# Kernel tuning notes

Measured on AMD Instinct MI355X. Metric: run time of the kernel, lower is better.

The kernel has to match this reference:

```python
import jax, jax.numpy as jnp
import numpy as np

B, N, E, H = 8, 2048, 1024, 16
D = E // H

def setup_inputs() -> dict:
    key = jax.random.key(0)
    kx, kw1, kb1, kw2, kb2 = jax.random.split(key, 5)
    scale = 0.02
    return {
        "x": jax.random.normal(kx, (B, N, E), dtype=jnp.float32),
        "Wqkv": jax.random.normal(kw1, (3 * E, E), dtype=jnp.float32) * scale,
        "bqkv": jax.random.normal(kb1, (3 * E,), dtype=jnp.float32) * scale,
        "Wo": jax.random.normal(kw2, (E, E), dtype=jnp.float32) * scale,
        "bo": jax.random.normal(kb2, (E,), dtype=jnp.float32) * scale,
    }

def reference(x, Wqkv, bqkv, Wo, bo):
    b, n, e = x.shape
    h, d = H, D
    # qkv projection: torch Linear is x @ W.T + b
    qkv = x @ Wqkv.T + bqkv                                   # [B,N,3E]
    qkv = qkv.reshape(b, n, 3, h, d).transpose(2, 0, 3, 1, 4)  # [3,B,H,N,D]
    q, k, v = qkv[0], qkv[1], qkv[2]                           # each [B,H,N,D]
    # NOTE: replicates the original's einsum labeling exactly: with q,k of
    # shape [B,H,N,D], 'nqhd,nkhd->nhqk' contracts over D and yields [B,N,H,H]
    # (softmax over the head axis), matching the torch source bit-for-bit.
    energy = jnp.einsum('nqhd,nkhd->nhqk', q, k)               # [B,N,H,H]
    attention = jax.nn.softmax(energy / jnp.sqrt(jnp.float32(e)), axis=-1)
    out = jnp.einsum('nhql,nlhd->nqhd', attention, v)          # [B,H,N,D]
    out = out.reshape(b, n, e)                                 # same raw-buffer reshape as torch
    return out @ Wo.T + bo
```

## Files before the change

kernel.cpp:

```cpp
#include <hip/hip_runtime.h>
#include <hip/hip_bf16.h>
#include <stdint.h>


typedef __attribute__((ext_vector_type(8))) short short8;
typedef __attribute__((ext_vector_type(8))) unsigned short ushort8;
typedef __attribute__((ext_vector_type(16))) float floatx16;

__device__ __forceinline__ unsigned short f2bf(float f) {
  union { float f; uint32_t u; } x; x.f = f;
  uint32_t u = x.u;
  return (unsigned short)((u + 0x7fffu + ((u >> 16) & 1u)) >> 16);
}
__device__ __forceinline__ float bf2f(unsigned short s) {
  union { uint32_t u; float f; } x; x.u = ((uint32_t)s) << 16; return x.f;
}
__device__ __forceinline__ void unpack8(uint4 u, float* f) {
  f[0] = bf2f((unsigned short)(u.x & 0xffffu)); f[1] = bf2f((unsigned short)(u.x >> 16));
  f[2] = bf2f((unsigned short)(u.y & 0xffffu)); f[3] = bf2f((unsigned short)(u.y >> 16));
  f[4] = bf2f((unsigned short)(u.z & 0xffffu)); f[5] = bf2f((unsigned short)(u.z >> 16));
  f[6] = bf2f((unsigned short)(u.w & 0xffffu)); f[7] = bf2f((unsigned short)(u.w >> 16));
}

__global__ __launch_bounds__(256) void cvt_all(const float* __restrict__ x,
                                               const float* __restrict__ w1,
                                               const float* __restrict__ w2,
                                               unsigned short* __restrict__ xb,
                                               unsigned short* __restrict__ w1b,
                                               unsigned short* __restrict__ w2b) {
  int i = blockIdx.x * 256 + threadIdx.x;
  const float* src;
  unsigned short* dst;
  if (i < 2097152) {
    src = x; dst = xb;
  } else if (i < 2097152 + 393216) {
    i -= 2097152; src = w1; dst = w1b;
  } else {
    i -= 2490368; src = w2; dst = w2b;
  }
  long base = (long)i * 8;
  const float4* p = (const float4*)(src + base);
  float4 a = p[0], b = p[1];
  ushort8 r;
  r[0] = f2bf(a.x); r[1] = f2bf(a.y); r[2] = f2bf(a.z); r[3] = f2bf(a.w);
  r[4] = f2bf(b.x); r[5] = f2bf(b.y); r[6] = f2bf(b.z); r[7] = f2bf(b.w);
  *(ushort8*)(dst + base) = r;
}

__device__ __forceinline__ void gl2lds16(const void* g, void* l) {
  __builtin_amdgcn_global_load_lds(
      (const uint32_t __attribute__((address_space(1)))*)g,
      (uint32_t __attribute__((address_space(3)))*)(uint32_t)(uintptr_t)l,
      16, 0, 0);
}

template <bool OUT_BF16>
__device__ __forceinline__ void gemm_core(const unsigned short* __restrict__ A,
                                          const unsigned short* __restrict__ Bm,
                                          const float* __restrict__ bias,
                                          void* __restrict__ Cout, int K,
                                          int ncols, int ldc) {
  const int id = blockIdx.x;
  const int local = id % (8 * ncols);
  const int brow = (id / (8 * ncols)) * 8 + (local & 7);
  const int bcol = local >> 3;

  __shared__ __align__(16) unsigned short lA[128 * 64];
  __shared__ __align__(16) unsigned short lB[128 * 64];
  const int tid = threadIdx.x;
  const int lane = tid & 63;
  const int wave = tid >> 6;
  const long row0 = (long)brow * 128;
  const long col0 = (long)bcol * 128;
  const int wr = (wave & 1) * 64;
  const int wc = (wave >> 1) * 64;
  const int l32 = lane & 31;
  const int lhi = lane >> 5;
  const int l7 = lane & 7;

  floatx16 acc[2][2] = {};

  const int rstage = tid >> 3;
  const int cstage = (tid & 7) ^ (rstage & 7);
  const unsigned short* gA0 = A + (row0 + rstage) * (long)K + cstage * 8;
  const unsigned short* gB0 = Bm + (col0 + rstage) * (long)K + cstage * 8;
  char* ldsA0 = (char*)lA + tid * 16;
  char* ldsB0 = (char*)lB + tid * 16;
  const long rowstep = (long)32 * K;

  int aRow[2], bRow[2], sOff[4];
#pragma unroll
  for (int i = 0; i < 2; i++) aRow[i] = (wr + i * 32 + l32) * 128;
#pragma unroll
  for (int j = 0; j < 2; j++) bRow[j] = (wc + j * 32 + l32) * 128;
#pragma unroll
  for (int s = 0; s < 4; s++) sOff[s] = ((2 * s + lhi) ^ l7) * 16;

  for (int k0 = 0; k0 < K; k0 += 64) {
    __syncthreads();
#pragma unroll
    for (int p = 0; p < 4; p++) {
      gl2lds16(gA0 + p * rowstep + k0, ldsA0 + p * 4096);
      gl2lds16(gB0 + p * rowstep + k0, ldsB0 + p * 4096);
    }
    __syncthreads();

#pragma unroll
    for (int s = 0; s < 4; s++) {
      short8 a0 = *(const short8*)((char*)lA + aRow[0] + sOff[s]);
      short8 a1 = *(const short8*)((char*)lA + aRow[1] + sOff[s]);
      short8 b0 = *(const short8*)((char*)lB + bRow[0] + sOff[s]);
      short8 b1 = *(const short8*)((char*)lB + bRow[1] + sOff[s]);
      acc[0][0] = __builtin_amdgcn_mfma_f32_32x32x16_bf16(a0, b0, acc[0][0], 0, 0, 0);
      acc[0][1] = __builtin_amdgcn_mfma_f32_32x32x16_bf16(a0, b1, acc[0][1], 0, 0, 0);
      acc[1][0] = __builtin_amdgcn_mfma_f32_32x32x16_bf16(a1, b0, acc[1][0], 0, 0, 0);
      acc[1][1] = __builtin_amdgcn_mfma_f32_32x32x16_bf16(a1, b1, acc[1][1], 0, 0, 0);
    }
  }

  float bv[2];
#pragma unroll
  for (int j = 0; j < 2; j++) bv[j] = bias[col0 + wc + j * 32 + l32];

#pragma unroll
  for (int i = 0; i < 2; i++) {
#pragma unroll
    for (int j = 0; j < 2; j++) {
      const long col = col0 + wc + j * 32 + l32;
      const long rbase = row0 + wr + i * 32 + 4 * lhi;
#pragma unroll
      for (int reg = 0; reg < 16; reg++) {
        const long row = rbase + (reg & 3) + 8 * (reg >> 2);
        float v = acc[i][j][reg] + bv[j];
        if (OUT_BF16)
          ((unsigned short*)Cout)[row * ldc + col] = f2bf(v);
        else
          ((float*)Cout)[row * ldc + col] = v;
      }
    }
  }
}

__global__ __launch_bounds__(256) void gemm_qkv(const unsigned short* __restrict__ A,
                                                const unsigned short* __restrict__ Bm,
                                                const float* __restrict__ bias,
                                                unsigned short* __restrict__ Cout, int K) {
  gemm_core<true>(A, Bm, bias, Cout, K, 24, 3072);
}
__global__ __launch_bounds__(256) void gemm_out(const unsigned short* __restrict__ A,
                                                const unsigned short* __restrict__ Bm,
                                                const float* __restrict__ bias,
                                                float* __restrict__ Cout, int K) {
  gemm_core<false>(A, Bm, bias, Cout, K, 8, 1024);
}

__global__ __launch_bounds__(256) void attn_kernel(const unsigned short* __restrict__ qkv,
                                                   unsigned short* __restrict__ out2) {
  __shared__ __align__(16) char lds[4 * 6144];
  const int tid = threadIdx.x;
  const int wave = tid >> 6;
  const int lane = tid & 63;
  const int token = blockIdx.x * 4 + wave;
  const int head = lane >> 2;
  const int sub = lane & 3;
  const int b = token >> 11;
  const int s = token & 2047;

  const char* gbase = (const char*)qkv + (long)token * 6144;
  char* lbase = lds + wave * 6144;
#pragma unroll
  for (int p = 0; p < 6; p++)
    gl2lds16(gbase + p * 1024 + lane * 16, lbase + p * 1024 + lane * 16);
  __syncthreads();

  float qf[16];
  {
    const uint4* qp = (const uint4*)(lbase + head * 128 + sub * 32);
    unpack8(qp[0], qf);
    unpack8(qp[1], qf + 8);
  }

  float e[16];
  const char* kbase = lbase + 2048 + sub * 32;
  for (int j = 0; j < 16; j++) {
    const uint4* kp = (const uint4*)(kbase + j * 128);
    float kf[16];
    unpack8(kp[0], kf);
    unpack8(kp[1], kf + 8);
    float a0 = 0.f, a1 = 0.f, a2 = 0.f, a3 = 0.f;
#pragma unroll
    for (int c = 0; c < 4; c++) {
      a0 += qf[c] * kf[c];
      a1 += qf[c + 4] * kf[c + 4];
      a2 += qf[c + 8] * kf[c + 8];
      a3 += qf[c + 12] * kf[c + 12];
    }
    float ej = (a0 + a1) + (a2 + a3);
    ej += __shfl_xor(ej, 1);
    ej += __shfl_xor(ej, 2);
    e[j] = ej * 0.03125f;
  }

  float mx = e[0];
#pragma unroll
  for (int j = 1; j < 16; j++) mx = fmaxf(mx, e[j]);
  float sum = 0.f;
#pragma unroll
  for (int j = 0; j < 16; j++) { e[j] = __expf(e[j] - mx); sum += e[j]; }
  const float inv = 1.f / sum;

  float o[16];
#pragma unroll
  for (int d = 0; d < 16; d++) o[d] = 0.f;
  const char* vbase = lbase + 4096 + sub * 32;
  for (int j = 0; j < 16; j++) {
    const float wgt = e[j] * inv;
    const uint4* vp = (const uint4*)(vbase + j * 128);
    float vf[16];
    unpack8(vp[0], vf);
    unpack8(vp[1], vf + 8);
#pragma unroll
    for (int d = 0; d < 16; d++) o[d] += wgt * vf[d];
  }

  const long row = (long)b * 2048 + head * 128 + (s >> 4);
  unsigned short* op = out2 + row * 1024 + (long)(s & 15) * 64 + sub * 16;
#pragma unroll
  for (int w = 0; w < 2; w++) {
    ushort8 r;
#pragma unroll
    for (int c = 0; c < 8; c++) r[c] = f2bf(o[w * 8 + c]);
    *(ushort8*)(op + w * 8) = r;
  }
}

extern "C" void kernel_launch(void* const* d_in, const int* in_sizes, int n_in,
                              void* d_out, int out_size, void* d_ws, size_t ws_size,
                              hipStream_t stream) {
  const float* x    = (const float*)d_in[0];
  const float* Wqkv = (const float*)d_in[1];
  const float* bqkv = (const float*)d_in[2];
  const float* Wo   = (const float*)d_in[3];
  const float* bo   = (const float*)d_in[4];
  float* out = (float*)d_out;

  char* ws = (char*)d_ws;
  unsigned short* x_bf    = (unsigned short*)(ws);
  unsigned short* wqkv_bf = (unsigned short*)(ws + 33554432);
  unsigned short* wo_bf   = (unsigned short*)(ws + 39845888);
  unsigned short* qkv_bf  = (unsigned short*)(ws + 41943040);
  unsigned short* out2_bf = (unsigned short*)(ws + 142606336);

  cvt_all<<<10240, 256, 0, stream>>>(x, Wqkv, Wo, x_bf, wqkv_bf, wo_bf);

  gemm_qkv<<<24 * 128, 256, 0, stream>>>(x_bf, wqkv_bf, bqkv, qkv_bf, 1024);

  attn_kernel<<<4096, 256, 0, stream>>>(qkv_bf, out2_bf);

  gemm_out<<<8 * 128, 256, 0, stream>>>(out2_bf, wo_bf, bo, out, 1024);
}
```

Baseline: 337.8 us.

## Rewrite GEMMs as 256x256 tiles with 4-stage LDS prefetch pipeline

Both projection GEMMs now use 256x256 output tiles with 512 threads and 16x16x32 MFMAs. A four-buffer LDS ring is filled by direct global-to-LDS loads three k-steps ahead, with explicit vmcnt waits, barriers and setprio around the MFMA clusters. The goal is more data reuse per tile and overlap of global loads with compute. The cost is 128KB of LDS per block and far fewer blocks (768 and 256), which risks poor CU occupancy and tail effects, especially for the output GEMM.

```diff
diff --git a/kernel.cpp b/kernel.cpp
--- a/kernel.cpp
+++ b/kernel.cpp
@@ -5,7 +5,7 @@
 
 typedef __attribute__((ext_vector_type(8))) short short8;
 typedef __attribute__((ext_vector_type(8))) unsigned short ushort8;
-typedef __attribute__((ext_vector_type(16))) float floatx16;
+typedef __attribute__((ext_vector_type(4))) float floatx4;
 
 __device__ __forceinline__ unsigned short f2bf(float f) {
   union { float f; uint32_t u; } x; x.f = f;
@@ -55,103 +55,145 @@
 }
 
 template <bool OUT_BF16>
-__device__ __forceinline__ void gemm_core(const unsigned short* __restrict__ A,
-                                          const unsigned short* __restrict__ Bm,
-                                          const float* __restrict__ bias,
-                                          void* __restrict__ Cout, int K,
-                                          int ncols, int ldc) {
+__device__ __forceinline__ void gemm256_core(const unsigned short* __restrict__ A,
+                                             const unsigned short* __restrict__ Bm,
+                                             const float* __restrict__ bias,
+                                             void* __restrict__ Cout,
+                                             int K, int ncols, int ldc) {
+  __shared__ __align__(16) char lds[131072];
+  char* lA = lds;
+  char* lB = lds + 65536;
+
   const int id = blockIdx.x;
   const int local = id % (8 * ncols);
   const int brow = (id / (8 * ncols)) * 8 + (local & 7);
   const int bcol = local >> 3;
-
-  __shared__ __align__(16) unsigned short lA[128 * 64];
-  __shared__ __align__(16) unsigned short lB[128 * 64];
+  const long row0 = (long)brow * 256;
+  const long col0 = (long)bcol * 256;
+
   const int tid = threadIdx.x;
   const int lane = tid & 63;
   const int wave = tid >> 6;
-  const long row0 = (long)brow * 128;
-  const long col0 = (long)bcol * 128;
-  const int wr = (wave & 1) * 64;
-  const int wc = (wave >> 1) * 64;
-  const int l32 = lane & 31;
-  const int lhi = lane >> 5;
-  const int l7 = lane & 7;
-
-  floatx16 acc[2][2] = {};
-
-  const int rstage = tid >> 3;
-  const int cstage = (tid & 7) ^ (rstage & 7);
-  const unsigned short* gA0 = A + (row0 + rstage) * (long)K + cstage * 8;
-  const unsigned short* gB0 = Bm + (col0 + rstage) * (long)K + cstage * 8;
-  char* ldsA0 = (char*)lA + tid * 16;
-  char* ldsB0 = (char*)lB + tid * 16;
-  const long rowstep = (long)32 * K;
-
-  int aRow[2], bRow[2], sOff[4];
-#pragma unroll
-  for (int i = 0; i < 2; i++) aRow[i] = (wr + i * 32 + l32) * 128;
-#pragma unroll
-  for (int j = 0; j < 2; j++) bRow[j] = (wc + j * 32 + l32) * 128;
-#pragma unroll
-  for (int s = 0; s < 4; s++) sOff[s] = ((2 * s + lhi) ^ l7) * 16;
-
-  for (int k0 = 0; k0 < K; k0 += 64) {
-    __syncthreads();
-#pragma unroll
-    for (int p = 0; p < 4; p++) {
-      gl2lds16(gA0 + p * rowstep + k0, ldsA0 + p * 4096);
-      gl2lds16(gB0 + p * rowstep + k0, ldsB0 + p * 4096);
+  const int wm = wave >> 2;
+  const int wn = wave & 3;
+  const int l15 = lane & 15;
+  const int lk = lane >> 4;
+
+  float bv[4];
+#pragma unroll
+  for (int n = 0; n < 4; ++n) bv[n] = bias[col0 + wn * 64 + n * 16 + l15];
+  asm volatile("s_waitcnt vmcnt(0)" ::: "memory");
+
+  const int trow = tid >> 2;
+  const int gch = (tid & 3) ^ ((tid >> 3) & 3);
+  const unsigned short* gA = A + (row0 + trow) * (long)K + gch * 8;
+  const unsigned short* gB = Bm + (col0 + trow) * (long)K + gch * 8;
+  const long rstep = (long)128 * K;
+  char* dA = lA + tid * 16;
+  char* dB = lB + tid * 16;
+
+  const int ch = ((lk ^ ((l15 >> 1) & 3)) << 4);
+  const int aoff = (wm * 128 + l15) * 64 + ch;
+  const int boff = (wn * 64 + l15) * 64 + ch;
+
+  floatx4 acc[8][4] = {};
+  const int NT = K >> 5;
+
+#pragma unroll
+  for (int t = 0; t < 3; ++t) {
+    const long ko = (long)t * 32;
+    gl2lds16(gA + ko, dA + t * 16384);
+    gl2lds16(gA + rstep + ko, dA + t * 16384 + 8192);
+    gl2lds16(gB + ko, dB + t * 16384);
+    gl2lds16(gB + rstep + ko, dB + t * 16384 + 8192);
+  }
+  asm volatile("s_waitcnt vmcnt(8)" ::: "memory");
+  __builtin_amdgcn_s_barrier();
+
+#pragma unroll 1
+  for (int kt = 0; kt < NT; ++kt) {
+    const char* bufA = lA + (kt & 3) * 16384;
+    const char* bufB = lB + (kt & 3) * 16384;
+    const bool stage = (kt + 3 < NT);
+    const long ko = (long)(kt + 3) * 32;
+    const int sb = ((kt + 3) & 3) * 16384;
+
+    short8 af[4], bfr[4];
+#pragma unroll
+    for (int m = 0; m < 4; ++m) af[m] = *(const short8*)(bufA + aoff + m * 1024);
+#pragma unroll
+    for (int n = 0; n < 4; ++n) bfr[n] = *(const short8*)(bufB + boff + n * 1024);
+    if (stage) {
+      gl2lds16(gA + ko, dA + sb);
+      gl2lds16(gA + rstep + ko, dA + sb + 8192);
     }
-    __syncthreads();
-
-#pragma unroll
-    for (int s = 0; s < 4; s++) {
-      short8 a0 = *(const short8*)((char*)lA + aRow[0] + sOff[s]);
-      short8 a1 = *(const short8*)((char*)lA + aRow[1] + sOff[s]);
-      short8 b0 = *(const short8*)((char*)lB + bRow[0] + sOff[s]);
-      short8 b1 = *(const short8*)((char*)lB + bRow[1] + sOff[s]);
-      acc[0][0] = __builtin_amdgcn_mfma_f32_32x32x16_bf16(a0, b0, acc[0][0], 0, 0, 0);
-      acc[0][1] = __builtin_amdgcn_mfma_f32_32x32x16_bf16(a0, b1, acc[0][1], 0, 0, 0);
-      acc[1][0] = __builtin_amdgcn_mfma_f32_32x32x16_bf16(a1, b0, acc[1][0], 0, 0, 0);
-      acc[1][1] = __builtin_amdgcn_mfma_f32_32x32x16_bf16(a1, b1, acc[1][1], 0, 0, 0);
+    __builtin_amdgcn_sched_barrier(0);
+    __builtin_amdgcn_s_barrier();
+    asm volatile("s_waitcnt lgkmcnt(0)" ::: "memory");
+    __builtin_amdgcn_sched_barrier(0);
+    __builtin_amdgcn_s_setprio(1);
+#pragma unroll
+    for (int m = 0; m < 4; ++m)
+#pragma unroll
+      for (int n = 0; n < 4; ++n)
+        acc[m][n] = __builtin_amdgcn_mfma_f32_16x16x32_bf16(af[m], bfr[n], acc[m][n], 0, 0, 0);
+    __builtin_amdgcn_s_setprio(0);
+    __builtin_amdgcn_sched_barrier(0);
+    __builtin_amdgcn_s_barrier();
+
+#pragma unroll
+    for (int m = 0; m < 4; ++m) af[m] = *(const short8*)(bufA + aoff + (m + 4) * 1024);
+    if (stage) {
+      gl2lds16(gB + ko, dB + sb);
+      gl2lds16(gB + rstep + ko, dB + sb + 8192);
     }
-  }
-
-  float bv[2];
-#pragma unroll
-  for (int j = 0; j < 2; j++) bv[j] = bias[col0 + wc + j * 32 + l32];
-
-#pragma unroll
-  for (int i = 0; i < 2; i++) {
-#pragma unroll
-    for (int j = 0; j < 2; j++) {
-      const long col = col0 + wc + j * 32 + l32;
-      const long rbase = row0 + wr + i * 32 + 4 * lhi;
-#pragma unroll
-      for (int reg = 0; reg < 16; reg++) {
-        const long row = rbase + (reg & 3) + 8 * (reg >> 2);
-        float v = acc[i][j][reg] + bv[j];
+    __builtin_amdgcn_sched_barrier(0);
+    __builtin_amdgcn_s_barrier();
+    asm volatile("s_waitcnt lgkmcnt(0)" ::: "memory");
+    __builtin_amdgcn_sched_barrier(0);
+    __builtin_amdgcn_s_setprio(1);
+#pragma unroll
+    for (int m = 0; m < 4; ++m)
+#pragma unroll
+      for (int n = 0; n < 4; ++n)
+        acc[m + 4][n] = __builtin_amdgcn_mfma_f32_16x16x32_bf16(af[m], bfr[n], acc[m + 4][n], 0, 0, 0);
+    __builtin_amdgcn_s_setprio(0);
+    __builtin_amdgcn_sched_barrier(0);
+    if (kt < NT - 3) { asm volatile("s_waitcnt vmcnt(8)" ::: "memory"); }
+    else if (kt == NT - 3) { asm volatile("s_waitcnt vmcnt(4)" ::: "memory"); }
+    else if (kt == NT - 2) { asm volatile("s_waitcnt vmcnt(0)" ::: "memory"); }
+    __builtin_amdgcn_s_barrier();
+  }
+
+  const long crow0 = row0 + wm * 128 + lk * 4;
+  const long ccol0 = col0 + wn * 64 + l15;
+#pragma unroll
+  for (int m = 0; m < 8; ++m)
+#pragma unroll
+    for (int n = 0; n < 4; ++n)
+#pragma unroll
+      for (int r = 0; r < 4; ++r) {
+        const long row = crow0 + m * 16 + r;
+        const long col = ccol0 + n * 16;
+        const float v = acc[m][n][r] + bv[n];
         if (OUT_BF16)
           ((unsigned short*)Cout)[row * ldc + col] = f2bf(v);
         else
           ((float*)Cout)[row * ldc + col] = v;
       }
-    }
-  }
-}
-
-__global__ __launch_bounds__(256) void gemm_qkv(const unsigned short* __restrict__ A,
-                                                const unsigned short* __restrict__ Bm,
-                                                const float* __restrict__ bias,
-                                                unsigned short* __restrict__ Cout, int K) {
-  gemm_core<true>(A, Bm, bias, Cout, K, 24, 3072);
-}
-__global__ __launch_bounds__(256) void gemm_out(const unsigned short* __restrict__ A,
-                                                const unsigned short* __restrict__ Bm,
-                                                const float* __restrict__ bias,
-                                                float* __restrict__ Cout, int K) {
-  gemm_core<false>(A, Bm, bias, Cout, K, 8, 1024);
+}
+
+__global__ __launch_bounds__(512, 2) void gemm_qkv(const unsigned short* __restrict__ A,
+                                                   const unsigned short* __restrict__ Bm,
+                                                   const float* __restrict__ bias,
+                                                   unsigned short* __restrict__ Cout, int K) {
+  gemm256_core<true>(A, Bm, bias, Cout, K, 12, 3072);
+}
+__global__ __launch_bounds__(512, 2) void gemm_out(const unsigned short* __restrict__ A,
+                                                   const unsigned short* __restrict__ Bm,
+                                                   const float* __restrict__ bias,
+                                                   float* __restrict__ Cout, int K) {
+  gemm256_core<false>(A, Bm, bias, Cout, K, 4, 1024);
 }
 
 __global__ __launch_bounds__(256) void attn_kernel(const unsigned short* __restrict__ qkv,
@@ -253,9 +295,9 @@
 
   cvt_all<<<10240, 256, 0, stream>>>(x, Wqkv, Wo, x_bf, wqkv_bf, wo_bf);
 
-  gemm_qkv<<<24 * 128, 256, 0, stream>>>(x_bf, wqkv_bf, bqkv, qkv_bf, 1024);
+  gemm_qkv<<<64 * 12, 512, 0, stream>>>(x_bf, wqkv_bf, bqkv, qkv_bf, 1024);
 
   attn_kernel<<<4096, 256, 0, stream>>>(qkv_bf, out2_bf);
 
-  gemm_out<<<8 * 128, 256, 0, stream>>>(out2_bf, wo_bf, bo, out, 1024);
-}
+  gemm_out<<<64 * 4, 512, 0, stream>>>(out2_bf, wo_bf, bo, out, 1024);
+}
```

New measurement: 322.3 us. 1.05x faster.
